# Performance work log

Measured on AMD Instinct MI355X. Metric: run time of the kernel, lower is better.

The kernel has to match this reference:

```python
import jax, jax.numpy as jnp
import numpy as np

N = 100000    # total nodes
E = 1600000   # total edges
B = 64        # graphs in batch
F_IN = 64     # node feature dim (input_shape)
F_E = 16      # edge feature dim (edge_shape)
A = 6         # action dim (action_shape)
H = 16        # hidden_channels
L = 4         # num GEN layers
EPS = 1e-7    # GENConv message eps


def _ln(x, g, b):
    mu = x.mean(-1, keepdims=True)
    var = x.var(-1, keepdims=True)
    return (x - mu) * jax.lax.rsqrt(var + 1e-5) * g + b


def _genconv(x, src, dst, ea, t, w1, b1, g1, be1, w2, b2):
    # GENConv with softmax aggregation: msg = relu(x_j + e) + eps,
    # alpha = scatter_softmax(t*msg, dst), aggr = scatter_sum(msg*alpha),
    # out = MLP(x + aggr) with MLP = Lin(H,2H) -> LN -> ReLU -> Lin(2H,H)
    msg = jax.nn.relu(x[src] + ea) + EPS                      # [E,H]
    z = t * msg
    m = jax.ops.segment_max(z, dst, num_segments=N)           # [N,H]
    e = jnp.exp(z - m[dst])
    s = jax.ops.segment_sum(e, dst, num_segments=N)
    alpha = e / (s[dst] + 1e-16)
    aggr = jax.ops.segment_sum(msg * alpha, dst, num_segments=N)
    h = x + aggr
    h = jax.nn.relu(_ln(h @ w1 + b1, g1, be1))
    return h @ w2 + b2


def setup_inputs() -> dict:
    key = jax.random.key(0)
    ks = jax.random.split(key, 20)
    def rn(k, shape, scale=0.1):
        return jax.random.normal(k, shape, dtype=jnp.float32) * scale
    return {
        "x": rn(ks[0], (N, F_IN), 1.0),
        "edge_attr": rn(ks[1], (E, F_E), 1.0),
        "edge_index": jax.random.randint(ks[2], (2, E), 0, N),
        "batch": (jnp.arange(N) * B) // N,  # sorted, every graph non-empty
        "action": rn(ks[3], (B, A), 1.0),
        "node_w": rn(ks[4], (F_IN, H)), "node_b": rn(ks[5], (H,)),
        "edge_w": rn(ks[6], (F_E, H)), "edge_b": rn(ks[7], (H,)),
        "t": jnp.ones((L,), jnp.float32),
        "mlp_w1": rn(ks[8], (L, H, 2 * H)), "mlp_b1": rn(ks[9], (L, 2 * H)),
        "mlp_g1": jnp.ones((L, 2 * H), jnp.float32),
        "mlp_be1": jnp.zeros((L, 2 * H), jnp.float32),
        "mlp_w2": rn(ks[10], (L, 2 * H, H)), "mlp_b2": rn(ks[11], (L, H)),
        "ln_g": jnp.ones((L, H), jnp.float32), "ln_b": jnp.zeros((L, H), jnp.float32),
        "pin_w": rn(ks[12], (2 * H, 128)), "pin_b": rn(ks[13], (128,)),
        "ph_w": rn(ks[14], (128 + A, 10)), "ph_b": rn(ks[15], (10,)),
        "po_w": rn(ks[16], (10, 1)), "po_b": rn(ks[17], (1,)),
    }


def reference(x, edge_attr, edge_index, batch, action, node_w, node_b, edge_w,
              edge_b, t, mlp_w1, mlp_b1, mlp_g1, mlp_be1, mlp_w2, mlp_b2,
              ln_g, ln_b, pin_w, pin_b, ph_w, ph_b, po_w, po_b):
    src, dst = edge_index[0], edge_index[1]
    h = x @ node_w + node_b
    ea = edge_attr @ edge_w + edge_b
    # layer 0: bare conv (as in original forward)
    h = _genconv(h, src, dst, ea, t[0], mlp_w1[0], mlp_b1[0], mlp_g1[0],
                 mlp_be1[0], mlp_w2[0], mlp_b2[0])
    # layers 1..3: DeepGCN 'res+' blocks: x + conv(relu(norm(x)))
    for i in range(1, L):
        y = jax.nn.relu(_ln(h, ln_g[i], ln_b[i]))
        h = h + _genconv(y, src, dst, ea, t[i], mlp_w1[i], mlp_b1[i],
                         mlp_g1[i], mlp_be1[i], mlp_w2[i], mlp_b2[i])
    # final norm + act from layer 0 (dropout disabled: eval mode)
    h = jax.nn.relu(_ln(h, ln_g[0], ln_b[0]))
    # global max + mean pooling per graph
    gmp = jax.ops.segment_max(h, batch, num_segments=B)
    cnt = jax.ops.segment_sum(jnp.ones((N, 1), h.dtype), batch, num_segments=B)
    gap = jax.ops.segment_sum(h, batch, num_segments=B) / cnt
    mol = jnp.concatenate([gmp, gap], axis=1)                 # [B, 32]
    fp = jax.nn.relu(mol @ pin_w + pin_b)                     # [B, 128]
    pol = jax.nn.relu(jnp.concatenate([fp, action], axis=1) @ ph_w + ph_b)
    return pol @ po_w + po_b                                  # [B, 1]
```

## Files before the change

### kernel.cpp

```cpp
#include <hip/hip_runtime.h>

#define N_NODES 100000
#define N_EDGES 1600000
#define NB 64
#define F_INn 64
#define HID 16
#define NL 4
#define NSCAN_BLK 391
#define NBIN 512
#define BINW 196
#define NPBLK 256
#define EPB (N_EDGES / NPBLK)

__global__ __launch_bounds__(256) void k_embed(
    const float* __restrict__ x, const float* __restrict__ nw,
    const float* __restrict__ nb, float* __restrict__ yout)
{
    __shared__ float xs[16 * 64];
    __shared__ float Wn[64 * 16];
    __shared__ float Bn[16];
    const int tid = threadIdx.x;
    for (int i = tid; i < 1024; i += 256) Wn[i] = nw[i];
    if (tid < 16) Bn[tid] = nb[tid];
    const int n0 = blockIdx.x * 16;
    reinterpret_cast<float4*>(xs)[tid] =
        reinterpret_cast<const float4*>(x + (size_t)n0 * F_INn)[tid];
    __syncthreads();
    const int nl = tid >> 4, j = tid & 15;
    float acc = Bn[j];
    #pragma unroll 8
    for (int k = 0; k < 64; ++k) acc += xs[nl * 64 + k] * Wn[k * 16 + j];
    yout[(size_t)(n0 + nl) * HID + j] = acc;
}

__global__ __launch_bounds__(256) void k_hist1(
    const int* __restrict__ dstA, int* __restrict__ histG)
{
    __shared__ int h[NBIN];
    const int tid = threadIdx.x, blk = blockIdx.x;
    for (int t = tid; t < NBIN; t += 256) h[t] = 0;
    __syncthreads();
    const int e0 = blk * EPB;
    for (int i = tid; i < EPB; i += 256)
        atomicAdd(&h[dstA[e0 + i] / BINW], 1);
    __syncthreads();
    for (int t = tid; t < NBIN; t += 256) histG[blk * NBIN + t] = h[t];
}

__global__ __launch_bounds__(256) void k_scanblk(
    const int* __restrict__ histG, int* __restrict__ boffsG,
    int* __restrict__ binTot)
{
    __shared__ int sc[NPBLK];
    const int tid = threadIdx.x, bin = blockIdx.x;
    const int v = histG[tid * NBIN + bin];
    sc[tid] = v;
    __syncthreads();
    for (int off = 1; off < NPBLK; off <<= 1) {
        int t = (tid >= off) ? sc[tid - off] : 0;
        __syncthreads();
        sc[tid] += t;
        __syncthreads();
    }
    boffsG[tid * NBIN + bin] = sc[tid] - v;
    if (tid == NPBLK - 1) binTot[bin] = sc[tid];
}

__global__ __launch_bounds__(512) void k_scanbin(
    const int* __restrict__ binTot, int* __restrict__ binStart)
{
    __shared__ int sc[NBIN];
    const int tid = threadIdx.x;
    const int v = binTot[tid];
    sc[tid] = v;
    __syncthreads();
    for (int off = 1; off < NBIN; off <<= 1) {
        int t = (tid >= off) ? sc[tid - off] : 0;
        __syncthreads();
        sc[tid] += t;
        __syncthreads();
    }
    binStart[tid] = sc[tid] - v;
    if (tid == NBIN - 1) binStart[NBIN] = sc[tid];
}

__global__ __launch_bounds__(256) void k_part(
    const int* __restrict__ dstA, const int* __restrict__ boffsG,
    const int* __restrict__ binStart, int2* __restrict__ part)
{
    __shared__ int cur[NBIN];
    const int tid = threadIdx.x, blk = blockIdx.x;
    for (int t = tid; t < NBIN; t += 256)
        cur[t] = binStart[t] + boffsG[blk * NBIN + t];
    __syncthreads();
    const int e0 = blk * EPB;
    for (int i = tid; i < EPB; i += 256) {
        const int e = e0 + i;
        const int d = dstA[e];
        const int p = atomicAdd(&cur[d / BINW], 1);
        part[p] = make_int2(d, e);
    }
}

__global__ __launch_bounds__(256) void k_cnt2(
    const int2* __restrict__ part, const int* __restrict__ binStart,
    int* __restrict__ cnt)
{
    __shared__ int h[BINW];
    const int tid = threadIdx.x, bin = blockIdx.x;
    const int base = bin * BINW;
    for (int t = tid; t < BINW; t += 256) h[t] = 0;
    __syncthreads();
    const int i0 = binStart[bin], i1 = binStart[bin + 1];
    for (int i = i0 + tid; i < i1; i += 256)
        atomicAdd(&h[part[i].x - base], 1);
    __syncthreads();
    for (int t = tid; t < BINW; t += 256) {
        const int idx = base + t;
        if (idx < N_NODES) cnt[idx] = h[t];
    }
}

__global__ __launch_bounds__(256) void k_scan1(
    const int* __restrict__ cnt, int* __restrict__ rowptr, int* __restrict__ bsum)
{
    __shared__ int sc[256];
    const int tid = threadIdx.x;
    const int i = blockIdx.x * 256 + tid;
    const int v = (i < N_NODES) ? cnt[i] : 0;
    sc[tid] = v;
    __syncthreads();
    for (int off = 1; off < 256; off <<= 1) {
        int t = (tid >= off) ? sc[tid - off] : 0;
        __syncthreads();
        sc[tid] += t;
        __syncthreads();
    }
    if (i < N_NODES) rowptr[i] = sc[tid] - v;
    if (tid == 255) bsum[blockIdx.x] = sc[tid];
}

__global__ __launch_bounds__(512) void k_scan2(
    const int* __restrict__ bsum, int* __restrict__ offs, int* __restrict__ rowptr)
{
    __shared__ int sc[512];
    const int tid = threadIdx.x;
    const int v = (tid < NSCAN_BLK) ? bsum[tid] : 0;
    sc[tid] = v;
    __syncthreads();
    for (int off = 1; off < 512; off <<= 1) {
        int t = (tid >= off) ? sc[tid - off] : 0;
        __syncthreads();
        sc[tid] += t;
        __syncthreads();
    }
    if (tid < NSCAN_BLK) offs[tid] = sc[tid] - v;
    if (tid == NSCAN_BLK - 1) rowptr[N_NODES] = sc[tid];
}

__global__ __launch_bounds__(256) void k_scan3(
    int* __restrict__ rowptr, const int* __restrict__ offs, int* __restrict__ cnt)
{
    const int i = blockIdx.x * 256 + threadIdx.x;
    if (i < N_NODES) {
        rowptr[i] += offs[i >> 8];
        cnt[i] = 0;
    }
}

__global__ __launch_bounds__(256) void k_place(
    const int2* __restrict__ part, const int* __restrict__ binStart,
    const int* __restrict__ rowptr, const int* __restrict__ srcA,
    const float* __restrict__ eattr, const float* __restrict__ ew,
    const float* __restrict__ ebv, int* __restrict__ srcP,
    float* __restrict__ eaP)
{
    __shared__ float EW[256];
    __shared__ float EB[16];
    __shared__ int cur[BINW];
    const int tid = threadIdx.x, bin = blockIdx.x;
    EW[tid] = ew[tid];
    if (tid < 16) EB[tid] = ebv[tid];
    const int base = bin * BINW;
    for (int t = tid; t < BINW; t += 256) {
        const int idx = base + t;
        cur[t] = (idx < N_NODES) ? rowptr[idx] : 0;
    }
    __syncthreads();
    const int i0 = binStart[bin], i1 = binStart[bin + 1];
    for (int i = i0 + tid; i < i1; i += 256) {
        const int2 de = part[i];
        const int p = atomicAdd(&cur[de.x - base], 1);
        const int e = de.y;
        srcP[p] = srcA[e];
        float a[16];
        {
            const float4* ag = reinterpret_cast<const float4*>(eattr + ((size_t)e << 4));
            *reinterpret_cast<float4*>(&a[0])  = ag[0];
            *reinterpret_cast<float4*>(&a[4])  = ag[1];
            *reinterpret_cast<float4*>(&a[8])  = ag[2];
            *reinterpret_cast<float4*>(&a[12]) = ag[3];
        }
        float acc[16];
        #pragma unroll
        for (int j = 0; j < 16; ++j) acc[j] = EB[j];
        #pragma unroll
        for (int k = 0; k < 16; ++k) {
            const float av = a[k];
            #pragma unroll
            for (int j = 0; j < 16; ++j) acc[j] += av * EW[k * 16 + j];
        }
        float4* eo = reinterpret_cast<float4*>(eaP + ((size_t)p << 4));
        eo[0] = make_float4(acc[0], acc[1], acc[2], acc[3]);
        eo[1] = make_float4(acc[4], acc[5], acc[6], acc[7]);
        eo[2] = make_float4(acc[8], acc[9], acc[10], acc[11]);
        eo[3] = make_float4(acc[12], acc[13], acc[14], acc[15]);
    }
}

__global__ __launch_bounds__(256) void k_count(
    const int* __restrict__ dstA, int* __restrict__ cnt)
{
    const int e = blockIdx.x * 256 + threadIdx.x;
    if (e < N_EDGES) atomicAdd(cnt + dstA[e], 1);
}

__global__ __launch_bounds__(256) void k_fill(
    const int* __restrict__ dstA, const int* __restrict__ rowptr,
    int* __restrict__ cnt, int* __restrict__ csr)
{
    const int e = blockIdx.x * 256 + threadIdx.x;
    if (e >= N_EDGES) return;
    const int d = dstA[e];
    const int pos = atomicAdd(cnt + d, 1);
    csr[rowptr[d] + pos] = e;
}

__global__ __launch_bounds__(256, 8) void k_aggr(
    const float* __restrict__ yin, const int* __restrict__ rowptr,
    const int* __restrict__ srcP, const float* __restrict__ eaP,
    const float* __restrict__ tArr, int layer, float* __restrict__ aggr)
{
    const int t = blockIdx.x * 256 + threadIdx.x;
    const int n = t >> 4;
    if (n >= N_NODES) return;
    const int sub = threadIdx.x & 15;
    const int es = sub >> 2, cg = sub & 3;
    const int row0 = rowptr[n], row1 = rowptr[n + 1];
    const float tv = tArr[layer];

    float4 s = make_float4(0.f, 0.f, 0.f, 0.f);
    float4 num = make_float4(0.f, 0.f, 0.f, 0.f);

    int i = row0 + es;
    bool has = (i < row1);
    int spn = 0;
    float4 ean = make_float4(0.f, 0.f, 0.f, 0.f);
    if (has) {
        spn = srcP[i];
        ean = reinterpret_cast<const float4*>(eaP + ((size_t)i << 4))[cg];
    }
    while (has) {
        const int sp = spn;
        const float4 ea = ean;
        const int i2 = i + 4;
        const bool has2 = (i2 < row1);
        if (has2) {
            spn = srcP[i2];
            ean = reinterpret_cast<const float4*>(eaP + ((size_t)i2 << 4))[cg];
        }
        const float4 yv = reinterpret_cast<const float4*>(yin + ((size_t)sp << 4))[cg];
        float m, ez;
        m = fmaxf(yv.x + ea.x, 0.f) + 1e-7f; ez = __expf(tv * m); s.x += ez; num.x += m * ez;
        m = fmaxf(yv.y + ea.y, 0.f) + 1e-7f; ez = __expf(tv * m); s.y += ez; num.y += m * ez;
        m = fmaxf(yv.z + ea.z, 0.f) + 1e-7f; ez = __expf(tv * m); s.z += ez; num.z += m * ez;
        m = fmaxf(yv.w + ea.w, 0.f) + 1e-7f; ez = __expf(tv * m); s.w += ez; num.w += m * ez;
        i = i2; has = has2;
    }
    s.x += __shfl_xor(s.x, 4); s.y += __shfl_xor(s.y, 4);
    s.z += __shfl_xor(s.z, 4); s.w += __shfl_xor(s.w, 4);
    num.x += __shfl_xor(num.x, 4); num.y += __shfl_xor(num.y, 4);
    num.z += __shfl_xor(num.z, 4); num.w += __shfl_xor(num.w, 4);
    s.x += __shfl_xor(s.x, 8); s.y += __shfl_xor(s.y, 8);
    s.z += __shfl_xor(s.z, 8); s.w += __shfl_xor(s.w, 8);
    num.x += __shfl_xor(num.x, 8); num.y += __shfl_xor(num.y, 8);
    num.z += __shfl_xor(num.z, 8); num.w += __shfl_xor(num.w, 8);
    if (es == 0) {
        float4 r;
        r.x = num.x / (s.x + 1e-16f);
        r.y = num.y / (s.y + 1e-16f);
        r.z = num.z / (s.z + 1e-16f);
        r.w = num.w / (s.w + 1e-16f);
        reinterpret_cast<float4*>(aggr + ((size_t)n << 4))[cg] = r;
    }
}

__global__ __launch_bounds__(256) void k_node(
    const float* __restrict__ yin, const float* __restrict__ hprev,
    const float* __restrict__ aggr,
    const float* __restrict__ w1, const float* __restrict__ b1,
    const float* __restrict__ g1, const float* __restrict__ be1,
    const float* __restrict__ w2, const float* __restrict__ b2,
    const float* __restrict__ gn, const float* __restrict__ bn,
    float* __restrict__ hout, float* __restrict__ yout, int layer)
{
    __shared__ float4 W1[128];
    __shared__ float4 W2[128];
    __shared__ float B1[32], G1[32], BE1[32], B2[16], GN[16], BN[16];
    const int tid = threadIdx.x;
    if (tid < 128) {
        W1[tid] = reinterpret_cast<const float4*>(w1)[tid];
        W2[tid] = reinterpret_cast<const float4*>(w2)[tid];
    }
    if (tid < 32) { B1[tid] = b1[tid]; G1[tid] = g1[tid]; BE1[tid] = be1[tid]; }
    if (tid < 16) { B2[tid] = b2[tid]; GN[tid] = gn[tid]; BN[tid] = bn[tid]; }
    __syncthreads();
    const int n = blockIdx.x * 256 + tid;
    if (n >= N_NODES) return;
    const size_t base = (size_t)n * HID;

    float hin[16];
    {
        const float4* yg = reinterpret_cast<const float4*>(yin + base);
        const float4* ag = reinterpret_cast<const float4*>(aggr + base);
        #pragma unroll
        for (int q = 0; q < 4; ++q) {
            float4 yv = yg[q], av = ag[q];
            hin[q * 4 + 0] = yv.x + av.x;
            hin[q * 4 + 1] = yv.y + av.y;
            hin[q * 4 + 2] = yv.z + av.z;
            hin[q * 4 + 3] = yv.w + av.w;
        }
    }
    float z[32];
    #pragma unroll
    for (int i = 0; i < 32; ++i) z[i] = B1[i];
    #pragma unroll
    for (int j = 0; j < 16; ++j) {
        const float hv = hin[j];
        #pragma unroll
        for (int q = 0; q < 8; ++q) {
            float4 w = W1[j * 8 + q];
            z[q * 4 + 0] += hv * w.x; z[q * 4 + 1] += hv * w.y;
            z[q * 4 + 2] += hv * w.z; z[q * 4 + 3] += hv * w.w;
        }
    }
    float mu = 0.f;
    #pragma unroll
    for (int i = 0; i < 32; ++i) mu += z[i];
    mu *= (1.f / 32.f);
    float var = 0.f;
    #pragma unroll
    for (int i = 0; i < 32; ++i) { float d = z[i] - mu; var += d * d; }
    var *= (1.f / 32.f);
    const float rs = rsqrtf(var + 1e-5f);

    float o[16];
    #pragma unroll
    for (int j = 0; j < 16; ++j) o[j] = B2[j];
    #pragma unroll
    for (int i = 0; i < 32; ++i) {
        const float r = fmaxf((z[i] - mu) * rs * G1[i] + BE1[i], 0.f);
        #pragma unroll
        for (int q = 0; q < 4; ++q) {
            float4 w = W2[i * 4 + q];
            o[q * 4 + 0] += r * w.x; o[q * 4 + 1] += r * w.y;
            o[q * 4 + 2] += r * w.z; o[q * 4 + 3] += r * w.w;
        }
    }
    float hn[16];
    if (layer == 0) {
        #pragma unroll
        for (int j = 0; j < 16; ++j) hn[j] = o[j];
    } else {
        const float4* hg = reinterpret_cast<const float4*>(hprev + base);
        float hr[16];
        *reinterpret_cast<float4*>(&hr[0])  = hg[0];
        *reinterpret_cast<float4*>(&hr[4])  = hg[1];
        *reinterpret_cast<float4*>(&hr[8])  = hg[2];
        *reinterpret_cast<float4*>(&hr[12]) = hg[3];
        #pragma unroll
        for (int j = 0; j < 16; ++j) hn[j] = hr[j] + o[j];
    }
    {
        float4* ho = reinterpret_cast<float4*>(hout + base);
        #pragma unroll
        for (int q = 0; q < 4; ++q)
            ho[q] = make_float4(hn[q*4+0], hn[q*4+1], hn[q*4+2], hn[q*4+3]);
    }
    float mu2 = 0.f;
    #pragma unroll
    for (int j = 0; j < 16; ++j) mu2 += hn[j];
    mu2 *= (1.f / 16.f);
    float v2 = 0.f;
    #pragma unroll
    for (int j = 0; j < 16; ++j) { float d = hn[j] - mu2; v2 += d * d; }
    v2 *= (1.f / 16.f);
    const float rs2 = rsqrtf(v2 + 1e-5f);
    float yn[16];
    #pragma unroll
    for (int j = 0; j < 16; ++j)
        yn[j] = fmaxf((hn[j] - mu2) * rs2 * GN[j] + BN[j], 0.f);
    {
        float4* yo = reinterpret_cast<float4*>(yout + base);
        #pragma unroll
        for (int q = 0; q < 4; ++q)
            yo[q] = make_float4(yn[q*4+0], yn[q*4+1], yn[q*4+2], yn[q*4+3]);
    }
}

__global__ __launch_bounds__(256) void k_layer(
    const float* __restrict__ yin, const float* __restrict__ hprev,
    const int* __restrict__ rowptr, const int* __restrict__ csr,
    const int* __restrict__ srcA, const float* __restrict__ eattr,
    const float* __restrict__ ew, const float* __restrict__ ebv,
    const float* __restrict__ tArr, int layer,
    const float* __restrict__ w1, const float* __restrict__ b1,
    const float* __restrict__ g1, const float* __restrict__ be1,
    const float* __restrict__ w2, const float* __restrict__ b2,
    const float* __restrict__ gn, const float* __restrict__ bn,
    float* __restrict__ hout, float* __restrict__ yout)
{
    __shared__ float EW[256];
    __shared__ float EB[16];
    __shared__ float4 W1[128];
    __shared__ float4 W2[128];
    __shared__ float B1[32], G1[32], BE1[32], B2[16], GN[16], BN[16];
    const int tid = threadIdx.x;
    EW[tid] = ew[tid];
    if (tid < 128) {
        W1[tid] = reinterpret_cast<const float4*>(w1)[tid];
        W2[tid] = reinterpret_cast<const float4*>(w2)[tid];
    }
    if (tid < 32) { B1[tid] = b1[tid]; G1[tid] = g1[tid]; BE1[tid] = be1[tid]; }
    if (tid < 16) { EB[tid] = ebv[tid]; B2[tid] = b2[tid]; GN[tid] = gn[tid]; BN[tid] = bn[tid]; }
    __syncthreads();

    const int t = blockIdx.x * 256 + tid;
    const int n = t >> 2, sub = t & 3;
    if (n >= N_NODES) return;
    const int row0 = rowptr[n], row1 = rowptr[n + 1];
    const float tv = tArr[layer];

    float s[16], num[16];
    #pragma unroll
    for (int j = 0; j < 16; ++j) { s[j] = 0.f; num[j] = 0.f; }

    for (int i = row0 + sub; i < row1; i += 4) {
        const int eid = csr[i];
        const int sp = srcA[eid];
        float a[16], yv[16];
        {
            const float4* ag = reinterpret_cast<const float4*>(eattr + (size_t)eid * 16);
            *reinterpret_cast<float4*>(&a[0])  = ag[0];
            *reinterpret_cast<float4*>(&a[4])  = ag[1];
            *reinterpret_cast<float4*>(&a[8])  = ag[2];
            *reinterpret_cast<float4*>(&a[12]) = ag[3];
            const float4* yg = reinterpret_cast<const float4*>(yin + (size_t)sp * 16);
            *reinterpret_cast<float4*>(&yv[0])  = yg[0];
            *reinterpret_cast<float4*>(&yv[4])  = yg[1];
            *reinterpret_cast<float4*>(&yv[8])  = yg[2];
            *reinterpret_cast<float4*>(&yv[12]) = yg[3];
        }
        float acc[16];
        #pragma unroll
        for (int j = 0; j < 16; ++j) acc[j] = EB[j];
        #pragma unroll
        for (int k = 0; k < 16; ++k) {
            const float av = a[k];
            #pragma unroll
            for (int j = 0; j < 16; ++j) acc[j] += av * EW[k * 16 + j];
        }
        #pragma unroll
        for (int j = 0; j < 16; ++j) {
            float m = fmaxf(yv[j] + acc[j], 0.f) + 1e-7f;
            float ez = __expf(tv * m);
            s[j] += ez;
            num[j] += m * ez;
        }
    }
    #pragma unroll
    for (int j = 0; j < 16; ++j) {
        s[j]   += __shfl_xor(s[j], 1);   num[j] += __shfl_xor(num[j], 1);
        s[j]   += __shfl_xor(s[j], 2);   num[j] += __shfl_xor(num[j], 2);
    }
    if (sub != 0) return;

    const size_t base = (size_t)n * HID;
    float hin[16];
    {
        const float4* yg = reinterpret_cast<const float4*>(yin + base);
        float yr[16];
        *reinterpret_cast<float4*>(&yr[0])  = yg[0];
        *reinterpret_cast<float4*>(&yr[4])  = yg[1];
        *reinterpret_cast<float4*>(&yr[8])  = yg[2];
        *reinterpret_cast<float4*>(&yr[12]) = yg[3];
        #pragma unroll
        for (int j = 0; j < 16; ++j) hin[j] = yr[j] + num[j] / (s[j] + 1e-16f);
    }
    float z[32];
    #pragma unroll
    for (int i = 0; i < 32; ++i) z[i] = B1[i];
    #pragma unroll
    for (int j = 0; j < 16; ++j) {
        const float hv = hin[j];
        #pragma unroll
        for (int q = 0; q < 8; ++q) {
            float4 w = W1[j * 8 + q];
            z[q * 4 + 0] += hv * w.x; z[q * 4 + 1] += hv * w.y;
            z[q * 4 + 2] += hv * w.z; z[q * 4 + 3] += hv * w.w;
        }
    }
    float mu = 0.f;
    #pragma unroll
    for (int i = 0; i < 32; ++i) mu += z[i];
    mu *= (1.f / 32.f);
    float var = 0.f;
    #pragma unroll
    for (int i = 0; i < 32; ++i) { float d = z[i] - mu; var += d * d; }
    var *= (1.f / 32.f);
    const float rs = rsqrtf(var + 1e-5f);

    float o[16];
    #pragma unroll
    for (int j = 0; j < 16; ++j) o[j] = B2[j];
    #pragma unroll
    for (int i = 0; i < 32; ++i) {
        const float r = fmaxf((z[i] - mu) * rs * G1[i] + BE1[i], 0.f);
        #pragma unroll
        for (int q = 0; q < 4; ++q) {
            float4 w = W2[i * 4 + q];
            o[q * 4 + 0] += r * w.x; o[q * 4 + 1] += r * w.y;
            o[q * 4 + 2] += r * w.z; o[q * 4 + 3] += r * w.w;
        }
    }
    float hn[16];
    if (layer == 0) {
        #pragma unroll
        for (int j = 0; j < 16; ++j) hn[j] = o[j];
    } else {
        const float4* hg = reinterpret_cast<const float4*>(hprev + base);
        float hr[16];
        *reinterpret_cast<float4*>(&hr[0])  = hg[0];
        *reinterpret_cast<float4*>(&hr[4])  = hg[1];
        *reinterpret_cast<float4*>(&hr[8])  = hg[2];
        *reinterpret_cast<float4*>(&hr[12]) = hg[3];
        #pragma unroll
        for (int j = 0; j < 16; ++j) hn[j] = hr[j] + o[j];
    }
    {
        float4* ho = reinterpret_cast<float4*>(hout + base);
        #pragma unroll
        for (int q = 0; q < 4; ++q)
            ho[q] = make_float4(hn[q*4+0], hn[q*4+1], hn[q*4+2], hn[q*4+3]);
    }
    float mu2 = 0.f;
    #pragma unroll
    for (int j = 0; j < 16; ++j) mu2 += hn[j];
    mu2 *= (1.f / 16.f);
    float v2 = 0.f;
    #pragma unroll
    for (int j = 0; j < 16; ++j) { float d = hn[j] - mu2; v2 += d * d; }
    v2 *= (1.f / 16.f);
    const float rs2 = rsqrtf(v2 + 1e-5f);
    float yn[16];
    #pragma unroll
    for (int j = 0; j < 16; ++j)
        yn[j] = fmaxf((hn[j] - mu2) * rs2 * GN[j] + BN[j], 0.f);
    {
        float4* yo = reinterpret_cast<float4*>(yout + base);
        #pragma unroll
        for (int q = 0; q < 4; ++q)
            yo[q] = make_float4(yn[q*4+0], yn[q*4+1], yn[q*4+2], yn[q*4+3]);
    }
}

__global__ __launch_bounds__(256) void k_pool(
    const float* __restrict__ y, const int* __restrict__ batch,
    float* __restrict__ gmax, float* __restrict__ gsum, float* __restrict__ gcnt)
{
    const int g = blockIdx.x;
    const int tid = threadIdx.x;
    int lo = 0, hi = N_NODES;
    while (lo < hi) { int mid = (lo + hi) >> 1; if (batch[mid] < g) lo = mid + 1; else hi = mid; }
    const int start = lo;
    lo = 0; hi = N_NODES;
    while (lo < hi) { int mid = (lo + hi) >> 1; if (batch[mid] < g + 1) lo = mid + 1; else hi = mid; }
    const int end = lo;

    const int ch = tid & 15, slot = tid >> 4;
    float mx = 0.f, sm = 0.f;
    for (int n = start + slot; n < end; n += 16) {
        float v = y[(size_t)n * HID + ch];
        mx = fmaxf(mx, v);
        sm += v;
    }
    __shared__ float rm[256], rsum[256];
    rm[tid] = mx; rsum[tid] = sm;
    __syncthreads();
    for (int off = 8; off >= 1; off >>= 1) {
        if (slot < off) {
            rm[tid] = fmaxf(rm[tid], rm[tid + off * 16]);
            rsum[tid] += rsum[tid + off * 16];
        }
        __syncthreads();
    }
    if (slot == 0) {
        gmax[g * HID + ch] = rm[ch];
        gsum[g * HID + ch] = rsum[ch];
        if (ch == 0) gcnt[g] = (float)(end - start);
    }
}

__global__ __launch_bounds__(128) void k_final(
    const float* __restrict__ gmax, const float* __restrict__ gsum,
    const float* __restrict__ gcnt, const float* __restrict__ action,
    const float* __restrict__ pin_w, const float* __restrict__ pin_b,
    const float* __restrict__ ph_w, const float* __restrict__ ph_b,
    const float* __restrict__ po_w, const float* __restrict__ po_b,
    float* __restrict__ out)
{
    __shared__ float mol[32];
    __shared__ float fpv[128];
    __shared__ float pol[10];
    const int b = blockIdx.x, tid = threadIdx.x;
    if (tid < 16) mol[tid] = gmax[b * 16 + tid];
    else if (tid < 32) mol[tid] = gsum[b * 16 + (tid - 16)] / gcnt[b];
    __syncthreads();
    float acc = pin_b[tid];
    #pragma unroll 4
    for (int k = 0; k < 32; ++k) acc += mol[k] * pin_w[k * 128 + tid];
    fpv[tid] = fmaxf(acc, 0.f);
    __syncthreads();
    if (tid < 10) {
        float a2 = ph_b[tid];
        for (int k = 0; k < 128; ++k) a2 += fpv[k] * ph_w[k * 10 + tid];
        #pragma unroll
        for (int k = 0; k < 6; ++k) a2 += action[b * 6 + k] * ph_w[(128 + k) * 10 + tid];
        pol[tid] = fmaxf(a2, 0.f);
    }
    __syncthreads();
    if (tid == 0) {
        float o = po_b[0];
        #pragma unroll
        for (int i = 0; i < 10; ++i) o += pol[i] * po_w[i];
        out[b] = o;
    }
}

extern "C" void kernel_launch(void* const* d_in, const int* in_sizes, int n_in,
                              void* d_out, int out_size, void* d_ws, size_t ws_size,
                              hipStream_t stream)
{
    const float* x       = (const float*)d_in[0];
    const float* eattr   = (const float*)d_in[1];
    const int*   eidx    = (const int*)d_in[2];
    const int*   batch   = (const int*)d_in[3];
    const float* action  = (const float*)d_in[4];
    const float* node_w  = (const float*)d_in[5];
    const float* node_b  = (const float*)d_in[6];
    const float* edge_w  = (const float*)d_in[7];
    const float* edge_b  = (const float*)d_in[8];
    const float* tArr    = (const float*)d_in[9];
    const float* mlp_w1  = (const float*)d_in[10];
    const float* mlp_b1  = (const float*)d_in[11];
    const float* mlp_g1  = (const float*)d_in[12];
    const float* mlp_be1 = (const float*)d_in[13];
    const float* mlp_w2  = (const float*)d_in[14];
    const float* mlp_b2  = (const float*)d_in[15];
    const float* ln_g    = (const float*)d_in[16];
    const float* ln_b    = (const float*)d_in[17];
    const float* pin_w   = (const float*)d_in[18];
    const float* pin_b   = (const float*)d_in[19];
    const float* ph_w    = (const float*)d_in[20];
    const float* ph_b    = (const float*)d_in[21];
    const float* po_w    = (const float*)d_in[22];
    const float* po_b    = (const float*)d_in[23];
    float* out = (float*)d_out;

    char* ws = (char*)d_ws;
    float* h      = (float*)ws;
    float* y      = h + (size_t)N_NODES * HID;
    float* aggr   = y + (size_t)N_NODES * HID;
    int*   cnt    = (int*)(aggr + (size_t)N_NODES * HID);
    int*   rowptr = cnt + N_NODES;
    int*   bsum   = rowptr + N_NODES + 1;
    int*   offs   = bsum + NSCAN_BLK;
    int*   csr    = offs + NSCAN_BLK + 1;
    float* gmax   = (float*)(csr + N_EDGES);
    float* gsum   = gmax + NB * HID;
    float* gcnt   = gsum + NB * HID;
    int*   srcP   = (int*)(gcnt + NB);
    float* eaP    = (float*)(srcP + N_EDGES);
    const size_t need = (size_t)((char*)(eaP + (size_t)N_EDGES * HID) - ws);
    const bool fast = (ws_size >= need);
    (void)in_sizes; (void)n_in; (void)out_size;

    int2* part    = (int2*)h;
    int*  histG   = (int*)aggr;
    int*  boffsG  = histG + NPBLK * NBIN;
    int*  binTot  = csr;
    int*  binStart= csr + NBIN;

    const int* srcA = eidx;
    const int* dstA = eidx + N_EDGES;

    if (fast) {
        k_hist1<<<NPBLK, 256, 0, stream>>>(dstA, histG);
        k_scanblk<<<NBIN, NPBLK, 0, stream>>>(histG, boffsG, binTot);
        k_scanbin<<<1, NBIN, 0, stream>>>(binTot, binStart);
        k_part<<<NPBLK, 256, 0, stream>>>(dstA, boffsG, binStart, part);
        k_cnt2<<<NBIN, 256, 0, stream>>>(part, binStart, cnt);
        k_scan1<<<NSCAN_BLK, 256, 0, stream>>>(cnt, rowptr, bsum);
        k_scan2<<<1, 512, 0, stream>>>(bsum, offs, rowptr);
        k_scan3<<<NSCAN_BLK, 256, 0, stream>>>(rowptr, offs, cnt);
        k_place<<<NBIN, 256, 0, stream>>>(part, binStart, rowptr, srcA,
            eattr, edge_w, edge_b, srcP, eaP);
        k_embed<<<N_NODES / 16, 256, 0, stream>>>(x, node_w, node_b, y);
        const int gridA = (16 * N_NODES + 255) / 256;
        const int gridN = (N_NODES + 255) / 256;
        for (int l = 0; l < NL; ++l) {
            const int nidx = (l < 3) ? (l + 1) : 0;
            k_aggr<<<gridA, 256, 0, stream>>>(y, rowptr, srcP, eaP, tArr, l, aggr);
            k_node<<<gridN, 256, 0, stream>>>(y, h, aggr,
                mlp_w1 + l * 512, mlp_b1 + l * 32, mlp_g1 + l * 32, mlp_be1 + l * 32,
                mlp_w2 + l * 512, mlp_b2 + l * 16, ln_g + nidx * 16, ln_b + nidx * 16,
                h, y, l);
        }
        k_pool<<<NB, 256, 0, stream>>>(y, batch, gmax, gsum, gcnt);
    } else {
        hipMemsetAsync(cnt, 0, (size_t)N_NODES * sizeof(int), stream);
        k_count<<<(N_EDGES + 255) / 256, 256, 0, stream>>>(dstA, cnt);
        k_scan1<<<NSCAN_BLK, 256, 0, stream>>>(cnt, rowptr, bsum);
        k_scan2<<<1, 512, 0, stream>>>(bsum, offs, rowptr);
        k_scan3<<<NSCAN_BLK, 256, 0, stream>>>(rowptr, offs, cnt);
        k_fill<<<(N_EDGES + 255) / 256, 256, 0, stream>>>(dstA, rowptr, cnt, csr);
        float* yA = y;
        float* yB = aggr;
        k_embed<<<N_NODES / 16, 256, 0, stream>>>(x, node_w, node_b, yA);
        const int grid = (4 * N_NODES + 255) / 256;
        for (int l = 0; l < NL; ++l) {
            const float* yin = (l & 1) ? yB : yA;
            float* yout      = (l & 1) ? yA : yB;
            const int nidx = (l < 3) ? (l + 1) : 0;
            k_layer<<<grid, 256, 0, stream>>>(
                yin, h, rowptr, csr, srcA, eattr, edge_w, edge_b, tArr, l,
                mlp_w1 + l * 512, mlp_b1 + l * 32, mlp_g1 + l * 32, mlp_be1 + l * 32,
                mlp_w2 + l * 512, mlp_b2 + l * 16, ln_g + nidx * 16, ln_b + nidx * 16,
                h, yout);
        }
        k_pool<<<NB, 256, 0, stream>>>(yA, batch, gmax, gsum, gcnt);
    }
    k_final<<<NB, 128, 0, stream>>>(gmax, gsum, gcnt, action,
        pin_w, pin_b, ph_w, ph_b, po_w, po_b, out);
}
```

Baseline: 423.2 us.

## Store edge embeddings in fp16 and fuse CSR build into per-bin rowptr

Edge embeddings are computed during partitioning and stored as half precision. The per-layer aggregation then reads half the bytes per edge and converts them back to float. The separate count, global scan and placement passes become a per-bin local histogram+scan kernel and a copy-placement kernel, which removes several launches. The cost is an extra fp16 staging buffer and reduced precision of the edge features.

```diff
diff --git a/kernel.cpp b/kernel.cpp
--- a/kernel.cpp
+++ b/kernel.cpp
@@ -1,4 +1,5 @@
 #include <hip/hip_runtime.h>
+#include <hip/hip_fp16.h>
 
 #define N_NODES 100000
 #define N_EDGES 1600000
@@ -12,6 +13,11 @@
 #define NPBLK 256
 #define EPB (N_EDGES / NPBLK)
 
+__device__ __forceinline__ unsigned pack2h(float a, float b) {
+    __half2 h = __floats2half2_rn(a, b);
+    return *reinterpret_cast<unsigned*>(&h);
+}
+
 __global__ __launch_bounds__(256) void k_embed(
     const float* __restrict__ x, const float* __restrict__ nw,
     const float* __restrict__ nb, float* __restrict__ yout)
@@ -84,12 +90,19 @@
     if (tid == NBIN - 1) binStart[NBIN] = sc[tid];
 }
 
-__global__ __launch_bounds__(256) void k_part(
-    const int* __restrict__ dstA, const int* __restrict__ boffsG,
-    const int* __restrict__ binStart, int2* __restrict__ part)
-{
+__global__ __launch_bounds__(256) void k_part2(
+    const int* __restrict__ dstA, const int* __restrict__ srcA,
+    const float* __restrict__ eattr, const float* __restrict__ ew,
+    const float* __restrict__ ebv, const int* __restrict__ boffsG,
+    const int* __restrict__ binStart, int* __restrict__ partD,
+    int* __restrict__ partS, __half* __restrict__ partE)
+{
+    __shared__ float EW[256];
+    __shared__ float EB[16];
     __shared__ int cur[NBIN];
     const int tid = threadIdx.x, blk = blockIdx.x;
+    EW[tid] = ew[tid];
+    if (tid < 16) EB[tid] = ebv[tid];
     for (int t = tid; t < NBIN; t += 256)
         cur[t] = binStart[t] + boffsG[blk * NBIN + t];
     __syncthreads();
@@ -97,102 +110,6 @@
     for (int i = tid; i < EPB; i += 256) {
         const int e = e0 + i;
         const int d = dstA[e];
-        const int p = atomicAdd(&cur[d / BINW], 1);
-        part[p] = make_int2(d, e);
-    }
-}
-
-__global__ __launch_bounds__(256) void k_cnt2(
-    const int2* __restrict__ part, const int* __restrict__ binStart,
-    int* __restrict__ cnt)
-{
-    __shared__ int h[BINW];
-    const int tid = threadIdx.x, bin = blockIdx.x;
-    const int base = bin * BINW;
-    for (int t = tid; t < BINW; t += 256) h[t] = 0;
-    __syncthreads();
-    const int i0 = binStart[bin], i1 = binStart[bin + 1];
-    for (int i = i0 + tid; i < i1; i += 256)
-        atomicAdd(&h[part[i].x - base], 1);
-    __syncthreads();
-    for (int t = tid; t < BINW; t += 256) {
-        const int idx = base + t;
-        if (idx < N_NODES) cnt[idx] = h[t];
-    }
-}
-
-__global__ __launch_bounds__(256) void k_scan1(
-    const int* __restrict__ cnt, int* __restrict__ rowptr, int* __restrict__ bsum)
-{
-    __shared__ int sc[256];
-    const int tid = threadIdx.x;
-    const int i = blockIdx.x * 256 + tid;
-    const int v = (i < N_NODES) ? cnt[i] : 0;
-    sc[tid] = v;
-    __syncthreads();
-    for (int off = 1; off < 256; off <<= 1) {
-        int t = (tid >= off) ? sc[tid - off] : 0;
-        __syncthreads();
-        sc[tid] += t;
-        __syncthreads();
-    }
-    if (i < N_NODES) rowptr[i] = sc[tid] - v;
-    if (tid == 255) bsum[blockIdx.x] = sc[tid];
-}
-
-__global__ __launch_bounds__(512) void k_scan2(
-    const int* __restrict__ bsum, int* __restrict__ offs, int* __restrict__ rowptr)
-{
-    __shared__ int sc[512];
-    const int tid = threadIdx.x;
-    const int v = (tid < NSCAN_BLK) ? bsum[tid] : 0;
-    sc[tid] = v;
-    __syncthreads();
-    for (int off = 1; off < 512; off <<= 1) {
-        int t = (tid >= off) ? sc[tid - off] : 0;
-        __syncthreads();
-        sc[tid] += t;
-        __syncthreads();
-    }
-    if (tid < NSCAN_BLK) offs[tid] = sc[tid] - v;
-    if (tid == NSCAN_BLK - 1) rowptr[N_NODES] = sc[tid];
-}
-
-__global__ __launch_bounds__(256) void k_scan3(
-    int* __restrict__ rowptr, const int* __restrict__ offs, int* __restrict__ cnt)
-{
-    const int i = blockIdx.x * 256 + threadIdx.x;
-    if (i < N_NODES) {
-        rowptr[i] += offs[i >> 8];
-        cnt[i] = 0;
-    }
-}
-
-__global__ __launch_bounds__(256) void k_place(
-    const int2* __restrict__ part, const int* __restrict__ binStart,
-    const int* __restrict__ rowptr, const int* __restrict__ srcA,
-    const float* __restrict__ eattr, const float* __restrict__ ew,
-    const float* __restrict__ ebv, int* __restrict__ srcP,
-    float* __restrict__ eaP)
-{
-    __shared__ float EW[256];
-    __shared__ float EB[16];
-    __shared__ int cur[BINW];
-    const int tid = threadIdx.x, bin = blockIdx.x;
-    EW[tid] = ew[tid];
-    if (tid < 16) EB[tid] = ebv[tid];
-    const int base = bin * BINW;
-    for (int t = tid; t < BINW; t += 256) {
-        const int idx = base + t;
-        cur[t] = (idx < N_NODES) ? rowptr[idx] : 0;
-    }
-    __syncthreads();
-    const int i0 = binStart[bin], i1 = binStart[bin + 1];
-    for (int i = i0 + tid; i < i1; i += 256) {
-        const int2 de = part[i];
-        const int p = atomicAdd(&cur[de.x - base], 1);
-        const int e = de.y;
-        srcP[p] = srcA[e];
         float a[16];
         {
             const float4* ag = reinterpret_cast<const float4*>(eattr + ((size_t)e << 4));
@@ -210,11 +127,73 @@
             #pragma unroll
             for (int j = 0; j < 16; ++j) acc[j] += av * EW[k * 16 + j];
         }
-        float4* eo = reinterpret_cast<float4*>(eaP + ((size_t)p << 4));
-        eo[0] = make_float4(acc[0], acc[1], acc[2], acc[3]);
-        eo[1] = make_float4(acc[4], acc[5], acc[6], acc[7]);
-        eo[2] = make_float4(acc[8], acc[9], acc[10], acc[11]);
-        eo[3] = make_float4(acc[12], acc[13], acc[14], acc[15]);
+        const int p = atomicAdd(&cur[d / BINW], 1);
+        partD[p] = d;
+        partS[p] = srcA[e];
+        uint4 lo, hi;
+        lo.x = pack2h(acc[0], acc[1]);   lo.y = pack2h(acc[2], acc[3]);
+        lo.z = pack2h(acc[4], acc[5]);   lo.w = pack2h(acc[6], acc[7]);
+        hi.x = pack2h(acc[8], acc[9]);   hi.y = pack2h(acc[10], acc[11]);
+        hi.z = pack2h(acc[12], acc[13]); hi.w = pack2h(acc[14], acc[15]);
+        uint4* eo = reinterpret_cast<uint4*>(partE) + ((size_t)p << 1);
+        eo[0] = lo;
+        eo[1] = hi;
+    }
+}
+
+__global__ __launch_bounds__(256) void k_rowptr(
+    const int* __restrict__ partD, const int* __restrict__ binStart,
+    int* __restrict__ rowptr)
+{
+    __shared__ int h[BINW];
+    __shared__ int sc[256];
+    const int tid = threadIdx.x, bin = blockIdx.x;
+    const int base = bin * BINW;
+    for (int t = tid; t < BINW; t += 256) h[t] = 0;
+    __syncthreads();
+    const int i0 = binStart[bin], i1 = binStart[bin + 1];
+    for (int i = i0 + tid; i < i1; i += 256)
+        atomicAdd(&h[partD[i] - base], 1);
+    __syncthreads();
+    const int v = (tid < BINW) ? h[tid] : 0;
+    sc[tid] = v;
+    __syncthreads();
+    for (int off = 1; off < 256; off <<= 1) {
+        int t = (tid >= off) ? sc[tid - off] : 0;
+        __syncthreads();
+        sc[tid] += t;
+        __syncthreads();
+    }
+    if (tid < BINW) {
+        const int idx = base + tid;
+        if (idx < N_NODES) rowptr[idx] = i0 + sc[tid] - v;
+    }
+    if (bin == NBIN - 1 && tid == 0) rowptr[N_NODES] = N_EDGES;
+}
+
+__global__ __launch_bounds__(256) void k_place2(
+    const int* __restrict__ partD, const int* __restrict__ partS,
+    const __half* __restrict__ partE, const int* __restrict__ binStart,
+    const int* __restrict__ rowptr, int* __restrict__ srcP,
+    __half* __restrict__ eaPh)
+{
+    __shared__ int cur[BINW];
+    const int tid = threadIdx.x, bin = blockIdx.x;
+    const int base = bin * BINW;
+    for (int t = tid; t < BINW; t += 256) {
+        const int idx = base + t;
+        cur[t] = (idx < N_NODES) ? rowptr[idx] : 0;
+    }
+    __syncthreads();
+    const int i0 = binStart[bin], i1 = binStart[bin + 1];
+    for (int i = i0 + tid; i < i1; i += 256) {
+        const int d = partD[i];
+        const int p = atomicAdd(&cur[d - base], 1);
+        srcP[p] = partS[i];
+        const uint4* si = reinterpret_cast<const uint4*>(partE) + ((size_t)i << 1);
+        uint4* di = reinterpret_cast<uint4*>(eaPh) + ((size_t)p << 1);
+        di[0] = si[0];
+        di[1] = si[1];
     }
 }
 
@@ -223,6 +202,53 @@
 {
     const int e = blockIdx.x * 256 + threadIdx.x;
     if (e < N_EDGES) atomicAdd(cnt + dstA[e], 1);
+}
+
+__global__ __launch_bounds__(256) void k_scan1(
+    const int* __restrict__ cnt, int* __restrict__ rowptr, int* __restrict__ bsum)
+{
+    __shared__ int sc[256];
+    const int tid = threadIdx.x;
+    const int i = blockIdx.x * 256 + tid;
+    const int v = (i < N_NODES) ? cnt[i] : 0;
+    sc[tid] = v;
+    __syncthreads();
+    for (int off = 1; off < 256; off <<= 1) {
+        int t = (tid >= off) ? sc[tid - off] : 0;
+        __syncthreads();
+        sc[tid] += t;
+        __syncthreads();
+    }
+    if (i < N_NODES) rowptr[i] = sc[tid] - v;
+    if (tid == 255) bsum[blockIdx.x] = sc[tid];
+}
+
+__global__ __launch_bounds__(512) void k_scan2(
+    const int* __restrict__ bsum, int* __restrict__ offs, int* __restrict__ rowptr)
+{
+    __shared__ int sc[512];
+    const int tid = threadIdx.x;
+    const int v = (tid < NSCAN_BLK) ? bsum[tid] : 0;
+    sc[tid] = v;
+    __syncthreads();
+    for (int off = 1; off < 512; off <<= 1) {
+        int t = (tid >= off) ? sc[tid - off] : 0;
+        __syncthreads();
+        sc[tid] += t;
+        __syncthreads();
+    }
+    if (tid < NSCAN_BLK) offs[tid] = sc[tid] - v;
+    if (tid == NSCAN_BLK - 1) rowptr[N_NODES] = sc[tid];
+}
+
+__global__ __launch_bounds__(256) void k_scan3(
+    int* __restrict__ rowptr, const int* __restrict__ offs, int* __restrict__ cnt)
+{
+    const int i = blockIdx.x * 256 + threadIdx.x;
+    if (i < N_NODES) {
+        rowptr[i] += offs[i >> 8];
+        cnt[i] = 0;
+    }
 }
 
 __global__ __launch_bounds__(256) void k_fill(
@@ -238,7 +264,7 @@
 
 __global__ __launch_bounds__(256, 8) void k_aggr(
     const float* __restrict__ yin, const int* __restrict__ rowptr,
-    const int* __restrict__ srcP, const float* __restrict__ eaP,
+    const int* __restrict__ srcP, const __half* __restrict__ eaPh,
     const float* __restrict__ tArr, int layer, float* __restrict__ aggr)
 {
     const int t = blockIdx.x * 256 + threadIdx.x;
@@ -255,26 +281,28 @@
     int i = row0 + es;
     bool has = (i < row1);
     int spn = 0;
-    float4 ean = make_float4(0.f, 0.f, 0.f, 0.f);
+    uint2 ean = make_uint2(0u, 0u);
     if (has) {
         spn = srcP[i];
-        ean = reinterpret_cast<const float4*>(eaP + ((size_t)i << 4))[cg];
+        ean = reinterpret_cast<const uint2*>(eaPh + ((size_t)i << 4))[cg];
     }
     while (has) {
         const int sp = spn;
-        const float4 ea = ean;
+        const uint2 eaw = ean;
         const int i2 = i + 4;
         const bool has2 = (i2 < row1);
         if (has2) {
             spn = srcP[i2];
-            ean = reinterpret_cast<const float4*>(eaP + ((size_t)i2 << 4))[cg];
+            ean = reinterpret_cast<const uint2*>(eaPh + ((size_t)i2 << 4))[cg];
         }
         const float4 yv = reinterpret_cast<const float4*>(yin + ((size_t)sp << 4))[cg];
+        const float2 f0 = __half22float2(*reinterpret_cast<const __half2*>(&eaw.x));
+        const float2 f1 = __half22float2(*reinterpret_cast<const __half2*>(&eaw.y));
         float m, ez;
-        m = fmaxf(yv.x + ea.x, 0.f) + 1e-7f; ez = __expf(tv * m); s.x += ez; num.x += m * ez;
-        m = fmaxf(yv.y + ea.y, 0.f) + 1e-7f; ez = __expf(tv * m); s.y += ez; num.y += m * ez;
-        m = fmaxf(yv.z + ea.z, 0.f) + 1e-7f; ez = __expf(tv * m); s.z += ez; num.z += m * ez;
-        m = fmaxf(yv.w + ea.w, 0.f) + 1e-7f; ez = __expf(tv * m); s.w += ez; num.w += m * ez;
+        m = fmaxf(yv.x + f0.x, 0.f) + 1e-7f; ez = __expf(tv * m); s.x += ez; num.x += m * ez;
+        m = fmaxf(yv.y + f0.y, 0.f) + 1e-7f; ez = __expf(tv * m); s.y += ez; num.y += m * ez;
+        m = fmaxf(yv.z + f1.x, 0.f) + 1e-7f; ez = __expf(tv * m); s.z += ez; num.z += m * ez;
+        m = fmaxf(yv.w + f1.y, 0.f) + 1e-7f; ez = __expf(tv * m); s.w += ez; num.w += m * ez;
         i = i2; has = has2;
     }
     s.x += __shfl_xor(s.x, 4); s.y += __shfl_xor(s.y, 4);
@@ -691,16 +719,18 @@
     float* gsum   = gmax + NB * HID;
     float* gcnt   = gsum + NB * HID;
     int*   srcP   = (int*)(gcnt + NB);
-    float* eaP    = (float*)(srcP + N_EDGES);
-    const size_t need = (size_t)((char*)(eaP + (size_t)N_EDGES * HID) - ws);
+    __half* eaPh  = (__half*)(srcP + N_EDGES);
+    __half* partE = eaPh + (size_t)N_EDGES * HID;
+    const size_t need = (size_t)((char*)(partE + (size_t)N_EDGES * HID) - ws);
     const bool fast = (ws_size >= need);
     (void)in_sizes; (void)n_in; (void)out_size;
 
-    int2* part    = (int2*)h;
-    int*  histG   = (int*)aggr;
-    int*  boffsG  = histG + NPBLK * NBIN;
-    int*  binTot  = csr;
-    int*  binStart= csr + NBIN;
+    int* partD    = (int*)h;
+    int* partS    = (int*)y;
+    int* histG    = (int*)aggr;
+    int* boffsG   = histG + NPBLK * NBIN;
+    int* binTot   = csr;
+    int* binStart = csr + NBIN;
 
     const int* srcA = eidx;
     const int* dstA = eidx + N_EDGES;
@@ -709,19 +739,17 @@
         k_hist1<<<NPBLK, 256, 0, stream>>>(dstA, histG);
         k_scanblk<<<NBIN, NPBLK, 0, stream>>>(histG, boffsG, binTot);
         k_scanbin<<<1, NBIN, 0, stream>>>(binTot, binStart);
-        k_part<<<NPBLK, 256, 0, stream>>>(dstA, boffsG, binStart, part);
-        k_cnt2<<<NBIN, 256, 0, stream>>>(part, binStart, cnt);
-        k_scan1<<<NSCAN_BLK, 256, 0, stream>>>(cnt, rowptr, bsum);
-        k_scan2<<<1, 512, 0, stream>>>(bsum, offs, rowptr);
-        k_scan3<<<NSCAN_BLK, 256, 0, stream>>>(rowptr, offs, cnt);
-        k_place<<<NBIN, 256, 0, stream>>>(part, binStart, rowptr, srcA,
-            eattr, edge_w, edge_b, srcP, eaP);
+        k_part2<<<NPBLK, 256, 0, stream>>>(dstA, srcA, eattr, edge_w, edge_b,
+            boffsG, binStart, partD, partS, partE);
+        k_rowptr<<<NBIN, 256, 0, stream>>>(partD, binStart, rowptr);
+        k_place2<<<NBIN, 256, 0, stream>>>(partD, partS, partE, binStart,
+            rowptr, srcP, eaPh);
         k_embed<<<N_NODES / 16, 256, 0, stream>>>(x, node_w, node_b, y);
         const int gridA = (16 * N_NODES + 255) / 256;
         const int gridN = (N_NODES + 255) / 256;
         for (int l = 0; l < NL; ++l) {
             const int nidx = (l < 3) ? (l + 1) : 0;
-            k_aggr<<<gridA, 256, 0, stream>>>(y, rowptr, srcP, eaP, tArr, l, aggr);
+            k_aggr<<<gridA, 256, 0, stream>>>(y, rowptr, srcP, eaPh, tArr, l, aggr);
             k_node<<<gridN, 256, 0, stream>>>(y, h, aggr,
                 mlp_w1 + l * 512, mlp_b1 + l * 32, mlp_g1 + l * 32, mlp_be1 + l * 32,
                 mlp_w2 + l * 512, mlp_b2 + l * 16, ln_g + nidx * 16, ln_b + nidx * 16,
```

After: 443.0 us. 4.7% more time.
